# Kernel tuning notes

Hardware: AMD Instinct MI355X
Metric: run time of the kernel (lower is better)

The kernel has to match this reference:

```python
import jax, jax.numpy as jnp
import numpy as np

TEMPERATURE = 1.0

def setup_inputs() -> dict:
    key = jax.random.key(0)
    k1, k2 = jax.random.split(key)
    B, I, O = 256, 1024, 1024
    x = jax.random.normal(k1, (B, I), dtype=jnp.float32)
    # mimic TruncatedNormal(stddev=1/sqrt(input_size)) init
    w = jax.random.normal(k2, (I, O), dtype=jnp.float32) * (1.0 / np.sqrt(I))
    b = jnp.zeros((O,), dtype=jnp.float32)
    return {"x": x, "w": w, "b": b}

def reference(x, w, b):
    # z: [B, I, O] outer product per sample
    z = jnp.einsum('bi,io->bio', x, w)
    n = x.shape[-1]
    # per-output-neuron temperature softmax over the input dim I
    s = jax.nn.softmax(jnp.abs(z) / TEMPERATURE, axis=1)
    out = n * jnp.sum(z * s, axis=1)  # [B, O]
    return out + b
```

## Files before the change

kernel.cpp:

```cpp
#include <hip/hip_runtime.h>

#define BDIM 256
#define IDIM 1024
#define ODIM 1024

#define TILE_O 64
#define TILE_B 2
#define NQ 4
#define QLEN (IDIM / NQ)

typedef float v2f __attribute__((ext_vector_type(2)));

#if __has_builtin(__builtin_amdgcn_exp2f)
#define FAST_EXP2(v) __builtin_amdgcn_exp2f(v)
#else
#define FAST_EXP2(v) exp2f(v)
#endif

__global__ __launch_bounds__(256, 8)
void stl_kernel(const float* __restrict__ x,
                const float* __restrict__ w,
                const float* __restrict__ bias,
                float* __restrict__ out) {
  __shared__ float xs[TILE_B][IDIM];
  __shared__ float ps[NQ][TILE_O][4];

  const int tx = threadIdx.x;
  const int ty = threadIdx.y;
  const int tid = ty * 64 + tx;
  const int o0 = blockIdx.x * TILE_O;
  const int b0 = blockIdx.y * TILE_B;

  const float LOG2E = 1.4426950408889634f;

#pragma unroll
  for (int k = 0; k < 2; ++k) {
    int f = tid + k * 256;
    int row = f >> 8;
    int col = f & 255;
    float4 v = ((const float4*)(x + (size_t)(b0 + row) * IDIM))[col];
    v.x *= LOG2E; v.y *= LOG2E; v.z *= LOG2E; v.w *= LOG2E;
    ((float4*)(&xs[row][0]))[col] = v;
  }
  __syncthreads();

  const int qbase = ty * QLEN;
  const float* wp = w + (size_t)qbase * ODIM + o0 + tx;

  v2f num = {0.0f, 0.0f};
  v2f den = {0.0f, 0.0f};

#pragma unroll 2
  for (int j = 0; j < QLEN; j += 8) {
    float wv[8];
#pragma unroll
    for (int u = 0; u < 8; ++u) wv[u] = wp[(size_t)(j + u) * ODIM];
    float4 xa0 = *(const float4*)(&xs[0][qbase + j]);
    float4 xa1 = *(const float4*)(&xs[0][qbase + j + 4]);
    float4 xb0 = *(const float4*)(&xs[1][qbase + j]);
    float4 xb1 = *(const float4*)(&xs[1][qbase + j + 4]);
    const float xa[8] = {xa0.x, xa0.y, xa0.z, xa0.w, xa1.x, xa1.y, xa1.z, xa1.w};
    const float xb[8] = {xb0.x, xb0.y, xb0.z, xb0.w, xb1.x, xb1.y, xb1.z, xb1.w};
#pragma unroll
    for (int u = 0; u < 8; ++u) {
      v2f p = {xa[u] * wv[u], xb[u] * wv[u]};
      v2f t;
      t.x = FAST_EXP2(__builtin_fabsf(p.x));
      t.y = FAST_EXP2(__builtin_fabsf(p.y));
      num += p * t;
      den += t;
    }
  }

  *(float4*)(&ps[ty][tx][0]) = make_float4(num.x, num.y, den.x, den.y);
  __syncthreads();

  if (ty == 0) {
    float4 a = *(const float4*)(&ps[0][tx][0]);
    float4 b = *(const float4*)(&ps[1][tx][0]);
    float4 c = *(const float4*)(&ps[2][tx][0]);
    float4 d = *(const float4*)(&ps[3][tx][0]);
    const float nx = a.x + b.x + c.x + d.x;
    const float ny = a.y + b.y + c.y + d.y;
    const float dx = a.z + b.z + c.z + d.z;
    const float dy = a.w + b.w + c.w + d.w;
    const float LN2 = 0.6931471805599453f;
    const float scale = (float)IDIM * LN2;
    const int o = o0 + tx;
    const float bo = bias[o];
    out[(size_t)b0 * ODIM + o] = scale * nx / dx + bo;
    out[(size_t)(b0 + 1) * ODIM + o] = scale * ny / dy + bo;
  }
}

extern "C" void kernel_launch(void* const* d_in, const int* in_sizes, int n_in,
                              void* d_out, int out_size, void* d_ws, size_t ws_size,
                              hipStream_t stream) {
  const float* x = (const float*)d_in[0];
  const float* w = (const float*)d_in[1];
  const float* b = (const float*)d_in[2];
  float* out = (float*)d_out;

  dim3 grid(ODIM / TILE_O, BDIM / TILE_B);
  dim3 block(64, 4);
  stl_kernel<<<grid, block, 0, stream>>>(x, w, b, out);
}
```

Baseline: 96.34 us.

## Process four batch rows per block with eight waves splitting the input dim

Raises the batch tile from 2 to 4 rows so each loaded weight value feeds four exp/accumulate chains instead of two. The input dimension is now split across 8 waves (512 threads) instead of 4, and the cross-wave reduction grows to match. This halves the grid and halves the total weight traffic from L2/global. The cost is larger blocks, more LDS for x, and a longer serial reduction in wave 0.

```diff
diff --git a/kernel.cpp b/kernel.cpp
--- a/kernel.cpp
+++ b/kernel.cpp
@@ -5,9 +5,9 @@
 #define ODIM 1024
 
 #define TILE_O 64
-#define TILE_B 2
-#define NQ 4
-#define QLEN (IDIM / NQ)
+#define TILE_B 4
+#define NW 8
+#define QLEN (IDIM / NW)
 
 typedef float v2f __attribute__((ext_vector_type(2)));
 
@@ -17,13 +17,13 @@
 #define FAST_EXP2(v) exp2f(v)
 #endif
 
-__global__ __launch_bounds__(256, 8)
+__global__ __launch_bounds__(512, 8)
 void stl_kernel(const float* __restrict__ x,
                 const float* __restrict__ w,
                 const float* __restrict__ bias,
                 float* __restrict__ out) {
   __shared__ float xs[TILE_B][IDIM];
-  __shared__ float ps[NQ][TILE_O][4];
+  __shared__ float ps[NW][TILE_O][8];
 
   const int tx = threadIdx.x;
   const int ty = threadIdx.y;
@@ -35,7 +35,7 @@
 
 #pragma unroll
   for (int k = 0; k < 2; ++k) {
-    int f = tid + k * 256;
+    int f = tid + k * 512;
     int row = f >> 8;
     int col = f & 255;
     float4 v = ((const float4*)(x + (size_t)(b0 + row) * IDIM))[col];
@@ -47,49 +47,56 @@
   const int qbase = ty * QLEN;
   const float* wp = w + (size_t)qbase * ODIM + o0 + tx;
 
-  v2f num = {0.0f, 0.0f};
-  v2f den = {0.0f, 0.0f};
+  v2f num01 = {0.0f, 0.0f}, num23 = {0.0f, 0.0f};
+  v2f den01 = {0.0f, 0.0f}, den23 = {0.0f, 0.0f};
 
 #pragma unroll 2
-  for (int j = 0; j < QLEN; j += 8) {
-    float wv[8];
+  for (int j = 0; j < QLEN; j += 4) {
+    float wv[4];
 #pragma unroll
-    for (int u = 0; u < 8; ++u) wv[u] = wp[(size_t)(j + u) * ODIM];
-    float4 xa0 = *(const float4*)(&xs[0][qbase + j]);
-    float4 xa1 = *(const float4*)(&xs[0][qbase + j + 4]);
-    float4 xb0 = *(const float4*)(&xs[1][qbase + j]);
-    float4 xb1 = *(const float4*)(&xs[1][qbase + j + 4]);
-    const float xa[8] = {xa0.x, xa0.y, xa0.z, xa0.w, xa1.x, xa1.y, xa1.z, xa1.w};
-    const float xb[8] = {xb0.x, xb0.y, xb0.z, xb0.w, xb1.x, xb1.y, xb1.z, xb1.w};
+    for (int u = 0; u < 4; ++u) wv[u] = wp[(size_t)(j + u) * ODIM];
+    float4 xq0 = *(const float4*)(&xs[0][qbase + j]);
+    float4 xq1 = *(const float4*)(&xs[1][qbase + j]);
+    float4 xq2 = *(const float4*)(&xs[2][qbase + j]);
+    float4 xq3 = *(const float4*)(&xs[3][qbase + j]);
+    const float x0[4] = {xq0.x, xq0.y, xq0.z, xq0.w};
+    const float x1[4] = {xq1.x, xq1.y, xq1.z, xq1.w};
+    const float x2[4] = {xq2.x, xq2.y, xq2.z, xq2.w};
+    const float x3[4] = {xq3.x, xq3.y, xq3.z, xq3.w};
 #pragma unroll
-    for (int u = 0; u < 8; ++u) {
-      v2f p = {xa[u] * wv[u], xb[u] * wv[u]};
-      v2f t;
-      t.x = FAST_EXP2(__builtin_fabsf(p.x));
-      t.y = FAST_EXP2(__builtin_fabsf(p.y));
-      num += p * t;
-      den += t;
+    for (int u = 0; u < 4; ++u) {
+      v2f p01 = {x0[u] * wv[u], x1[u] * wv[u]};
+      v2f p23 = {x2[u] * wv[u], x3[u] * wv[u]};
+      v2f t01, t23;
+      t01.x = FAST_EXP2(__builtin_fabsf(p01.x));
+      t01.y = FAST_EXP2(__builtin_fabsf(p01.y));
+      t23.x = FAST_EXP2(__builtin_fabsf(p23.x));
+      t23.y = FAST_EXP2(__builtin_fabsf(p23.y));
+      num01 += p01 * t01; den01 += t01;
+      num23 += p23 * t23; den23 += t23;
     }
   }
 
-  *(float4*)(&ps[ty][tx][0]) = make_float4(num.x, num.y, den.x, den.y);
+  *(float4*)(&ps[ty][tx][0]) = make_float4(num01.x, num01.y, num23.x, num23.y);
+  *(float4*)(&ps[ty][tx][4]) = make_float4(den01.x, den01.y, den23.x, den23.y);
   __syncthreads();
 
   if (ty == 0) {
-    float4 a = *(const float4*)(&ps[0][tx][0]);
-    float4 b = *(const float4*)(&ps[1][tx][0]);
-    float4 c = *(const float4*)(&ps[2][tx][0]);
-    float4 d = *(const float4*)(&ps[3][tx][0]);
-    const float nx = a.x + b.x + c.x + d.x;
-    const float ny = a.y + b.y + c.y + d.y;
-    const float dx = a.z + b.z + c.z + d.z;
-    const float dy = a.w + b.w + c.w + d.w;
+    float n[4] = {0, 0, 0, 0}, d[4] = {0, 0, 0, 0};
+#pragma unroll
+    for (int q = 0; q < NW; ++q) {
+      float4 a = *(const float4*)(&ps[q][tx][0]);
+      float4 b = *(const float4*)(&ps[q][tx][4]);
+      n[0] += a.x; n[1] += a.y; n[2] += a.z; n[3] += a.w;
+      d[0] += b.x; d[1] += b.y; d[2] += b.z; d[3] += b.w;
+    }
     const float LN2 = 0.6931471805599453f;
     const float scale = (float)IDIM * LN2;
     const int o = o0 + tx;
     const float bo = bias[o];
-    out[(size_t)b0 * ODIM + o] = scale * nx / dx + bo;
-    out[(size_t)(b0 + 1) * ODIM + o] = scale * ny / dy + bo;
+#pragma unroll
+    for (int r = 0; r < 4; ++r)
+      out[(size_t)(b0 + r) * ODIM + o] = scale * n[r] / d[r] + bo;
   }
 }
 
@@ -102,6 +109,6 @@
   float* out = (float*)d_out;
 
   dim3 grid(ODIM / TILE_O, BDIM / TILE_B);
-  dim3 block(64, 4);
+  dim3 block(64, NW);
   stl_kernel<<<grid, block, 0, stream>>>(x, w, b, out);
 }
```

After: 95.14 us. No clear change (-1.2%).
